# Kernel tuning notes

Hardware: AMD Instinct MI355X
Metric: run time of the kernel (lower is better)

Reference implementation:

```python
import jax, jax.numpy as jnp
import numpy as np

B, N, F_IN = 32, 1024, 128
DIM, NUM_HEAD = 16, 8
D = DIM * NUM_HEAD  # 128


def setup_inputs() -> dict:
    key = jax.random.key(0)
    ks = jax.random.split(key, 8)
    atom_query = jax.random.normal(ks[0], (B, N, F_IN), dtype=jnp.float32)
    mask = (jax.random.uniform(ks[1], (B, N, 1)) < 0.9).astype(jnp.float32)
    s = 1.0 / np.sqrt(F_IN)
    Wq = jax.random.normal(ks[2], (F_IN, D), dtype=jnp.float32) * s
    bq = jnp.zeros((D,), dtype=jnp.float32)
    Wk = jax.random.normal(ks[3], (F_IN, D), dtype=jnp.float32) * s
    bk = jnp.zeros((D,), dtype=jnp.float32)
    Wv = jax.random.normal(ks[4], (F_IN, D), dtype=jnp.float32) * s
    bv = jnp.zeros((D,), dtype=jnp.float32)
    return {"atom_query": atom_query, "mask": mask,
            "Wq": Wq, "bq": bq, "Wk": Wk, "bk": bk, "Wv": Wv, "bv": bv}


def reference(atom_query, mask, Wq, bq, Wk, bk, Wv, bv):
    scale = 0.5  # self.scale
    q = atom_query @ Wq + bq            # [B, N, D]
    k = atom_query @ Wk + bk            # [B, N, D]
    v = atom_query @ Wv + bv            # [B, N, D] (v_proj=True)
    dk = jnp.asarray(q.shape[-1], jnp.float32) ** (-scale)
    q = q * dk
    energy = jnp.einsum('bqd,bkd->bqk', q, k)      # [B, N, N]
    energy = mask * energy                          # mask broadcasts over k
    agg = jnp.sum(energy, axis=-1, keepdims=True)   # [B, N, 1]
    agg = mask * agg
    # norm=False branch skipped
    agg = agg + (1.0 - mask) * (-1e9)
    attn = jax.nn.softmax(agg, axis=1)              # softmax over query axis
    context = jnp.sum(mask * (attn * v), axis=1)    # [B, D]
    return attn, context
```

## Files before the change

kernel.cpp:

```cpp
#include <hip/hip_runtime.h>

#define B    32
#define N    1024
#define FIN  128
#define CHN  16
#define ROWS 64
#define GRID (B * CHN)

#define OFF_PASUM 0
#define OFF_P     (B * CHN * FIN)
#define OFF_WPART (OFF_P + B * N)
#define OFF_M     (OFF_WPART + B * CHN * FIN)
#define OFF_L     (OFF_M + B * CHN)
#define OFF_S     (OFF_L + B * CHN)

__global__ __launch_bounds__(256) void k_asum(const float* __restrict__ aq,
                                              float* __restrict__ ws) {
    const int b = blockIdx.x >> 4, ch = blockIdx.x & 15;
    const float4* g4 = (const float4*)aq + ((size_t)b * N + ch * ROWS) * 32;
    float4 acc = make_float4(0.f, 0.f, 0.f, 0.f);
    #pragma unroll
    for (int i = 0; i < 8; ++i) {
        float4 v = g4[i * 256 + threadIdx.x];
        acc.x += v.x; acc.y += v.y; acc.z += v.z; acc.w += v.w;
    }
    __shared__ float4 sh[256];
    sh[threadIdx.x] = acc;
    __syncthreads();
    if (threadIdx.x < 32) {
        float4 r = sh[threadIdx.x];
        #pragma unroll
        for (int g = 1; g < 8; ++g) {
            float4 t = sh[g * 32 + threadIdx.x];
            r.x += t.x; r.y += t.y; r.z += t.z; r.w += t.w;
        }
        float4* outp = (float4*)(ws + OFF_PASUM) + (b * CHN + ch) * 32;
        outp[threadIdx.x] = r;
    }
}

__global__ __launch_bounds__(256) void k_main(
    const float* __restrict__ aq, const float* __restrict__ mask,
    const float* __restrict__ Wq, const float* __restrict__ bq,
    const float* __restrict__ Wk, const float* __restrict__ bk,
    float* __restrict__ ws)
{
    const int b = blockIdx.x >> 4, ch = blockIdx.x & 15;
    const int tid = threadIdx.x, f = tid & 127, h = tid >> 7;

    __shared__ float tile[ROWS * FIN];
    __shared__ float red[256];
    __shared__ float asum_s[FIN], ksum_s[FIN], u_s[FIN], mp_s[ROWS];
    __shared__ float c_sh;

    float4 stage[8];
    const float4* g4 = (const float4*)aq + ((size_t)b * N + ch * ROWS) * 32;
    #pragma unroll
    for (int i = 0; i < 8; ++i) stage[i] = g4[i * 256 + tid];

    {
        float a = 0.f;
        #pragma unroll
        for (int c = 0; c < 8; ++c)
            a += ws[OFF_PASUM + (b * CHN + h * 8 + c) * FIN + f];
        red[tid] = a;
    }
    __syncthreads();
    if (tid < FIN) asum_s[f] = red[f] + red[f + 128];
    __syncthreads();
    {
        float ks = 0.f;
        #pragma unroll 8
        for (int i = 0; i < 64; ++i) {
            int fi = h * 64 + i;
            ks += asum_s[fi] * Wk[fi * FIN + f];
        }
        red[tid] = ks;
    }
    __syncthreads();
    if (tid < FIN) ksum_s[f] = red[f] + red[f + 128] + 1024.f * bk[f];
    __syncthreads();
    {
        float uu = 0.f;
        #pragma unroll 8
        for (int i = 0; i < 64; ++i) {
            int d = h * 64 + i;
            uu += Wq[f * FIN + d] * ksum_s[d];
        }
        red[tid] = uu;
    }
    __syncthreads();
    if (tid < FIN) u_s[f] = red[f] + red[f + 128];
    if (tid < 64) {
        float cc = bq[tid] * ksum_s[tid] + bq[tid + 64] * ksum_s[tid + 64];
        #pragma unroll
        for (int off = 32; off > 0; off >>= 1) cc += __shfl_xor(cc, off);
        if (tid == 0) c_sh = cc;
    }
    {
        float4* t4 = (float4*)tile;
        #pragma unroll
        for (int i = 0; i < 8; ++i) {
            int g = i * 256 + tid;
            int row = g >> 5, c4 = g & 31;
            t4[row * 32 + (c4 ^ (row & 31))] = stage[i];
        }
    }
    __syncthreads();

    {
        const int r = tid & 63, q = tid >> 6;
        const float4* t4 = (const float4*)tile;
        const float4* u4 = (const float4*)u_s;
        float acc = 0.f;
        #pragma unroll
        for (int jj = 0; jj < 8; ++jj) {
            int j = q * 8 + jj;
            float4 a = t4[r * 32 + (j ^ (r & 31))];
            float4 uu = u4[j];
            acc += a.x * uu.x + a.y * uu.y + a.z * uu.z + a.w * uu.w;
        }
        red[tid] = acc;
    }
    __syncthreads();
    if (tid < ROWS) {
        const float dkc = 0.08838834764831845f;
        float dot = red[tid] + red[tid + 64] + red[tid + 128] + red[tid + 192];
        float m = mask[b * N + ch * ROWS + tid];
        float raw = dkc * (dot + c_sh);
        float aggv = m * raw + (1.f - m) * (-1e9f);
        float Mc = aggv;
        #pragma unroll
        for (int off = 32; off > 0; off >>= 1) Mc = fmaxf(Mc, __shfl_xor(Mc, off));
        float p = __expf(aggv - Mc);
        float mp = m * p;
        ws[OFF_P + b * N + ch * ROWS + tid] = p;
        mp_s[tid] = mp;
        float Lc = p, Sc = mp;
        #pragma unroll
        for (int off = 32; off > 0; off >>= 1) {
            Lc += __shfl_xor(Lc, off);
            Sc += __shfl_xor(Sc, off);
        }
        if (tid == 0) {
            ws[OFF_M + b * CHN + ch] = Mc;
            ws[OFF_L + b * CHN + ch] = Lc;
            ws[OFF_S + b * CHN + ch] = Sc;
        }
    }
    __syncthreads();
    {
        float w = 0.f;
        #pragma unroll 8
        for (int i = 0; i < 32; ++i) {
            int r = h * 32 + i;
            w += mp_s[r] * tile[r * FIN + ((((f >> 2) ^ (r & 31)) << 2) | (f & 3))];
        }
        red[tid] = w;
    }
    __syncthreads();
    if (tid < FIN)
        ws[OFF_WPART + (b * CHN + ch) * FIN + f] = red[f] + red[f + 128];
}

__global__ __launch_bounds__(256) void k_final(const float* __restrict__ Wv,
                                               const float* __restrict__ bv,
                                               const float* __restrict__ ws,
                                               float* __restrict__ out) {
    const int b = blockIdx.x >> 2, sub = blockIdx.x & 3;
    const int tid = threadIdx.x, f = tid & 127, h = tid >> 7;
    float M = -3.0e38f;
    #pragma unroll
    for (int c = 0; c < CHN; ++c) M = fmaxf(M, ws[OFF_M + b * CHN + c]);
    float Em[CHN], L = 0.f, S = 0.f;
    #pragma unroll
    for (int c = 0; c < CHN; ++c) {
        float e = __expf(ws[OFF_M + b * CHN + c] - M);
        Em[c] = e;
        L += e * ws[OFF_L + b * CHN + c];
        S += e * ws[OFF_S + b * CHN + c];
    }
    const float invL = 1.f / L;
    {
        int n = sub * 256 + tid;
        out[b * N + n] = ws[OFF_P + b * N + n] * Em[sub * 4 + (tid >> 6)] * invL;
    }
    if (sub != 0) return;
    __shared__ float wsh[FIN];
    __shared__ float red[256];
    {
        float w = 0.f;
        #pragma unroll
        for (int c = 0; c < 8; ++c)
            w += Em[h * 8 + c] * ws[OFF_WPART + (b * CHN + h * 8 + c) * FIN + f];
        red[tid] = w;
    }
    __syncthreads();
    if (tid < FIN) wsh[f] = red[f] + red[f + 128];
    __syncthreads();
    {
        float ctx = 0.f;
        #pragma unroll 8
        for (int i = 0; i < 64; ++i) {
            int fi = h * 64 + i;
            ctx += wsh[fi] * Wv[fi * FIN + f];
        }
        red[tid] = ctx;
    }
    __syncthreads();
    if (tid < FIN)
        out[B * N + b * FIN + f] = (red[f] + red[f + 128]) * invL + S * invL * bv[f];
}

extern "C" void kernel_launch(void* const* d_in, const int* in_sizes, int n_in,
                              void* d_out, int out_size, void* d_ws, size_t ws_size,
                              hipStream_t stream) {
    const float* aq   = (const float*)d_in[0];
    const float* mask = (const float*)d_in[1];
    const float* Wq   = (const float*)d_in[2];
    const float* bq   = (const float*)d_in[3];
    const float* Wk   = (const float*)d_in[4];
    const float* bk   = (const float*)d_in[5];
    const float* Wv   = (const float*)d_in[6];
    const float* bv   = (const float*)d_in[7];
    float* ws  = (float*)d_ws;
    float* out = (float*)d_out;

    k_asum <<<GRID,  256, 0, stream>>>(aq, ws);
    k_main <<<GRID,  256, 0, stream>>>(aq, mask, Wq, bq, Wk, bk, ws);
    k_final<<<B * 4, 256, 0, stream>>>(Wv, bv, ws, out);
}
```

Baseline: 99.88 us.

## Precompute Wq·Wkᵀ Gram matrix in the asum kernel to shorten k_main's serial chain

Adds 32 blocks to the asum kernel that compute G = Wq·Wkᵀ together with the bias terms (Wq·bk, bq·Wk, bq·bk), storing them in workspace. k_main then forms u with one matvec of asum against G instead of two dependent matvecs through Wk and Wq, which removes one barrier-separated stage per block. In exchange the first kernel does extra weight work, and the extra blocks doing 128-long serial dot products may lengthen that kernel's tail.

```diff
diff --git a/kernel.cpp b/kernel.cpp
--- a/kernel.cpp
+++ b/kernel.cpp
@@ -6,6 +6,7 @@
 #define CHN  16
 #define ROWS 64
 #define GRID (B * CHN)
+#define GRID_A (GRID + 32)
 
 #define OFF_PASUM 0
 #define OFF_P     (B * CHN * FIN)
@@ -13,44 +14,84 @@
 #define OFF_M     (OFF_WPART + B * CHN * FIN)
 #define OFF_L     (OFF_M + B * CHN)
 #define OFF_S     (OFF_L + B * CHN)
-
-__global__ __launch_bounds__(256) void k_asum(const float* __restrict__ aq,
-                                              float* __restrict__ ws) {
-    const int b = blockIdx.x >> 4, ch = blockIdx.x & 15;
-    const float4* g4 = (const float4*)aq + ((size_t)b * N + ch * ROWS) * 32;
-    float4 acc = make_float4(0.f, 0.f, 0.f, 0.f);
-    #pragma unroll
-    for (int i = 0; i < 8; ++i) {
-        float4 v = g4[i * 256 + threadIdx.x];
-        acc.x += v.x; acc.y += v.y; acc.z += v.z; acc.w += v.w;
-    }
-    __shared__ float4 sh[256];
-    sh[threadIdx.x] = acc;
-    __syncthreads();
-    if (threadIdx.x < 32) {
-        float4 r = sh[threadIdx.x];
-        #pragma unroll
-        for (int g = 1; g < 8; ++g) {
-            float4 t = sh[g * 32 + threadIdx.x];
-            r.x += t.x; r.y += t.y; r.z += t.z; r.w += t.w;
-        }
-        float4* outp = (float4*)(ws + OFF_PASUM) + (b * CHN + ch) * 32;
-        outp[threadIdx.x] = r;
-    }
-}
-
-__global__ __launch_bounds__(256) void k_main(
-    const float* __restrict__ aq, const float* __restrict__ mask,
+#define OFF_GT    (OFF_S + B * CHN)
+#define OFF_G0    (OFF_GT + FIN * FIN)
+#define OFF_EV    (OFF_G0 + FIN)
+#define OFF_C0    (OFF_EV + FIN)
+
+__global__ __launch_bounds__(256) void k_asum_pre(
+    const float* __restrict__ aq,
     const float* __restrict__ Wq, const float* __restrict__ bq,
     const float* __restrict__ Wk, const float* __restrict__ bk,
     float* __restrict__ ws)
 {
+    const int tid = threadIdx.x;
+    __shared__ float4 sh[256];
+    if (blockIdx.x < GRID) {
+        const int b = blockIdx.x >> 4, ch = blockIdx.x & 15;
+        const float4* g4 = (const float4*)aq + ((size_t)b * N + ch * ROWS) * 32;
+        float4 acc = make_float4(0.f, 0.f, 0.f, 0.f);
+        #pragma unroll
+        for (int i = 0; i < 8; ++i) {
+            float4 v = g4[i * 256 + tid];
+            acc.x += v.x; acc.y += v.y; acc.z += v.z; acc.w += v.w;
+        }
+        sh[tid] = acc;
+        __syncthreads();
+        if (tid < 32) {
+            float4 r = sh[tid];
+            #pragma unroll
+            for (int g = 1; g < 8; ++g) {
+                float4 t = sh[g * 32 + tid];
+                r.x += t.x; r.y += t.y; r.z += t.z; r.w += t.w;
+            }
+            float4* outp = (float4*)(ws + OFF_PASUM) + (b * CHN + ch) * 32;
+            outp[tid] = r;
+        }
+        return;
+    }
+    const int gb = blockIdx.x - GRID;
+    const int f = tid & 127, half = tid >> 7;
+    #pragma unroll
+    for (int j = 0; j < 2; ++j) {
+        const int e = gb * 4 + half * 2 + j;
+        float acc = 0.f;
+        #pragma unroll 8
+        for (int d = 0; d < FIN; ++d)
+            acc += Wq[f * FIN + d] * Wk[e * FIN + d];
+        ws[OFF_GT + e * FIN + f] = acc;
+    }
+    if (gb == 31) {
+        if (half == 0) {
+            float g = 0.f;
+            #pragma unroll 8
+            for (int d = 0; d < FIN; ++d) g += Wq[f * FIN + d] * bk[d];
+            ws[OFF_G0 + f] = 1024.f * g;
+        } else {
+            float ev = 0.f;
+            #pragma unroll 8
+            for (int d = 0; d < FIN; ++d) ev += bq[d] * Wk[f * FIN + d];
+            ws[OFF_EV + f] = ev;
+        }
+        if (tid < 64) {
+            float cc = bq[tid] * bk[tid] + bq[tid + 64] * bk[tid + 64];
+            #pragma unroll
+            for (int off = 32; off > 0; off >>= 1) cc += __shfl_xor(cc, off);
+            if (tid == 0) ws[OFF_C0] = 1024.f * cc;
+        }
+    }
+}
+
+__global__ __launch_bounds__(256) void k_main(
+    const float* __restrict__ aq, const float* __restrict__ mask,
+    float* __restrict__ ws)
+{
     const int b = blockIdx.x >> 4, ch = blockIdx.x & 15;
     const int tid = threadIdx.x, f = tid & 127, h = tid >> 7;
 
     __shared__ float tile[ROWS * FIN];
     __shared__ float red[256];
-    __shared__ float asum_s[FIN], ksum_s[FIN], u_s[FIN], mp_s[ROWS];
+    __shared__ float asum_s[FIN], u_s[FIN], mp_s[ROWS];
     __shared__ float c_sh;
 
     float4 stage[8];
@@ -69,33 +110,22 @@
     if (tid < FIN) asum_s[f] = red[f] + red[f + 128];
     __syncthreads();
     {
-        float ks = 0.f;
+        float uu = 0.f;
         #pragma unroll 8
         for (int i = 0; i < 64; ++i) {
-            int fi = h * 64 + i;
-            ks += asum_s[fi] * Wk[fi * FIN + f];
-        }
-        red[tid] = ks;
-    }
-    __syncthreads();
-    if (tid < FIN) ksum_s[f] = red[f] + red[f + 128] + 1024.f * bk[f];
-    __syncthreads();
-    {
-        float uu = 0.f;
-        #pragma unroll 8
-        for (int i = 0; i < 64; ++i) {
-            int d = h * 64 + i;
-            uu += Wq[f * FIN + d] * ksum_s[d];
+            int e = h * 64 + i;
+            uu += asum_s[e] * ws[OFF_GT + e * FIN + f];
         }
         red[tid] = uu;
     }
     __syncthreads();
-    if (tid < FIN) u_s[f] = red[f] + red[f + 128];
+    if (tid < FIN) u_s[f] = red[f] + red[f + 128] + ws[OFF_G0 + f];
     if (tid < 64) {
-        float cc = bq[tid] * ksum_s[tid] + bq[tid + 64] * ksum_s[tid + 64];
+        float cc = ws[OFF_EV + tid] * asum_s[tid]
+                 + ws[OFF_EV + tid + 64] * asum_s[tid + 64];
         #pragma unroll
         for (int off = 32; off > 0; off >>= 1) cc += __shfl_xor(cc, off);
-        if (tid == 0) c_sh = cc;
+        if (tid == 0) c_sh = cc + ws[OFF_C0];
     }
     {
         float4* t4 = (float4*)tile;
@@ -226,7 +256,7 @@
     float* ws  = (float*)d_ws;
     float* out = (float*)d_out;
 
-    k_asum <<<GRID,  256, 0, stream>>>(aq, ws);
-    k_main <<<GRID,  256, 0, stream>>>(aq, mask, Wq, bq, Wk, bk, ws);
-    k_final<<<B * 4, 256, 0, stream>>>(Wv, bv, ws, out);
-}
+    k_asum_pre<<<GRID_A, 256, 0, stream>>>(aq, Wq, bq, Wk, bk, ws);
+    k_main    <<<GRID,   256, 0, stream>>>(aq, mask, ws);
+    k_final   <<<B * 4,  256, 0, stream>>>(Wv, bv, ws, out);
+}
```

New measurement: 109.7 us. 9.8% more time.
